# Performance work log

Measured on AMD Instinct MI355X. Metric: run time of the kernel, lower is better.

The kernel has to match this reference:

```python
import jax, jax.numpy as jnp
import numpy as np

N, E, D, K = 50000, 600000, 128, 8
EPS = 1e-09


def setup_inputs() -> dict:
    key = jax.random.key(0)
    ks = jax.random.split(key, 10)
    feature = jax.random.normal(ks[0], (N, D), dtype=jnp.float32)
    snorm_n = jax.random.uniform(ks[1], (N, 1), dtype=jnp.float32)
    src = jax.random.randint(ks[2], (E,), 0, N, dtype=jnp.int32)
    dst = jax.random.randint(ks[3], (E,), 0, N, dtype=jnp.int32)
    W_low = jax.random.normal(ks[4], (D, D), dtype=jnp.float32) / np.sqrt(D)
    W_high = jax.random.normal(ks[5], (D, D), dtype=jnp.float32) / np.sqrt(D)
    W_mid = jax.random.normal(ks[6], (D, D), dtype=jnp.float32) / np.sqrt(D)
    gamma_low = jax.random.uniform(ks[7], (K,), dtype=jnp.float32)
    gamma_high = jax.random.uniform(ks[8], (K,), dtype=jnp.float32)
    gamma_mid = jax.random.uniform(ks[9], (K,), dtype=jnp.float32)
    bias = jnp.zeros((D,), dtype=jnp.float32)
    return {"feature": feature, "snorm_n": snorm_n, "src": src, "dst": dst,
            "W_low": W_low, "W_high": W_high, "W_mid": W_mid,
            "gamma_low": gamma_low, "gamma_high": gamma_high,
            "gamma_mid": gamma_mid, "bias": bias}


def _mp(feat, src, dst, norm):
    # symmetric-normalized SpMM: h[v] = norm[v] * sum_{u->v} norm[u]*feat[u]
    msg = (feat * norm[:, None])[src]                        # [E, D] gather
    agg = jax.ops.segment_sum(msg, dst, num_segments=N)       # [N, D] scatter-add
    return agg * norm[:, None]


def reference(feature, snorm_n, src, dst, W_low, W_high, W_mid,
              gamma_low, gamma_high, gamma_mid, bias):
    deg = jax.ops.segment_sum(jnp.ones((E,), feature.dtype), dst, num_segments=N)
    norm = jnp.clip(deg, 1.0) ** -0.5                          # in-degree^-0.5
    alpha = jnp.linspace(EPS, 1.0 - EPS, K).astype(feature.dtype)
    midalpha = jnp.linspace(EPS, 1.0, K).astype(feature.dtype)

    h = _mp(feature, src, dst, norm)

    gl = jax.nn.relu(gamma_low)
    o0 = (jnp.dot(alpha, gl) * h + jnp.dot(1.0 - alpha, gl) * feature) @ W_low.T
    gh = jax.nn.relu(gamma_high)
    o1 = (jnp.dot(-alpha, gh) * h + jnp.dot(1.0 - alpha, gh) * feature) @ W_high.T
    gm = jax.nn.relu(gamma_mid)
    h1 = _mp(h, src, dst, norm)
    o2 = (jnp.sum(gm) * h1 - jnp.dot(midalpha, gm) * feature) @ W_mid.T

    # sequential mutual gating, exactly as the torch in-place updates
    o0 = o0 * jax.nn.sigmoid(o1 + o2)
    o1 = o1 * jax.nn.sigmoid(o0 + o2)
    o2 = o2 * jax.nn.sigmoid(o0 + o1)

    out = o0 + o1 + o2 + bias
    out = out * snorm_n          # graph_norm
    out = jax.nn.relu(out)       # activation
    return out
```

## Files before the change

kernel.cpp:

```cpp
#include <hip/hip_runtime.h>
#include <hip/hip_bf16.h>
#include <math.h>

#define N_NODES 50000
#define N_EDGES 600000
#define DIM 128
#define KGAM 8
#define EPSV 1e-9f

typedef __attribute__((ext_vector_type(8))) short short8;
typedef __attribute__((ext_vector_type(4))) float float4v;

__device__ __forceinline__ float bf2f(short s) {
    unsigned int u = ((unsigned int)(unsigned short)s) << 16;
    return __builtin_bit_cast(float, u);
}
__device__ __forceinline__ short f2bf(float f) {
    return (short)__builtin_bit_cast(unsigned short, __float2bfloat16(f));
}
__device__ __forceinline__ unsigned int pack2(float a, float b) {
    return (unsigned int)(unsigned short)f2bf(a) | ((unsigned int)(unsigned short)f2bf(b) << 16);
}
__device__ __forceinline__ float sigm(float x) { return 1.f / (1.f + __expf(-x)); }

__global__ void k_zero_int(int* __restrict__ p, int n) {
    int i = blockIdx.x * blockDim.x + threadIdx.x;
    if (i < n) p[i] = 0;
}

__global__ void k_deg(const int* __restrict__ dst, int* __restrict__ deg) {
    int e = blockIdx.x * blockDim.x + threadIdx.x;
    if (e < N_EDGES) atomicAdd(&deg[dst[e]], 1);
}

__global__ void k_scan1(const int* __restrict__ deg, int* __restrict__ rowstart,
                        int* __restrict__ bsums, float* __restrict__ norm) {
    __shared__ int s[256];
    int tid = threadIdx.x;
    int i0 = blockIdx.x * 1024 + tid * 4;
    int v[4]; int sum = 0;
#pragma unroll
    for (int c = 0; c < 4; ++c) {
        int i = i0 + c;
        int d = (i < N_NODES) ? deg[i] : 0;
        v[c] = d; sum += d;
    }
    s[tid] = sum; __syncthreads();
#pragma unroll
    for (int off = 1; off < 256; off <<= 1) {
        int t = (tid >= off) ? s[tid - off] : 0;
        __syncthreads();
        s[tid] += t;
        __syncthreads();
    }
    if (tid == 255) bsums[blockIdx.x] = s[255];
    int run = s[tid] - sum;
#pragma unroll
    for (int c = 0; c < 4; ++c) {
        int i = i0 + c;
        if (i < N_NODES) {
            rowstart[i] = run;
            norm[i] = rsqrtf((float)(v[c] < 1 ? 1 : v[c]));
        }
        run += v[c];
    }
}

__global__ void k_scan2(int* __restrict__ bsums, int nb) {
    __shared__ int s[64];
    int tid = threadIdx.x;
    int v = (tid < nb) ? bsums[tid] : 0;
    s[tid] = v; __syncthreads();
#pragma unroll
    for (int off = 1; off < 64; off <<= 1) {
        int t = (tid >= off) ? s[tid - off] : 0;
        __syncthreads();
        s[tid] += t;
        __syncthreads();
    }
    if (tid < nb) bsums[tid] = s[tid] - v;
}

__global__ void k_scan3(const int* __restrict__ bsums, int* __restrict__ rowstart) {
    int i = blockIdx.x * blockDim.x + threadIdx.x;
    if (i < N_NODES) rowstart[i] += bsums[i >> 10];
    if (i == 0) rowstart[N_NODES] = N_EDGES;
}

__global__ void k_fill(const int* __restrict__ src, const int* __restrict__ dst,
                       const int* __restrict__ rowstart, int* __restrict__ cnt,
                       int* __restrict__ esrc) {
    int e = blockIdx.x * blockDim.x + threadIdx.x;
    if (e < N_EDGES) {
        int d = dst[e];
        int slot = rowstart[d] + atomicAdd(&cnt[d], 1);
        esrc[slot] = src[e];
    }
}

__global__ void k_coeffs(const float* __restrict__ gl, const float* __restrict__ gh,
                         const float* __restrict__ gm, float* __restrict__ c) {
    if (threadIdx.x == 0 && blockIdx.x == 0) {
        float a0 = 0, b0 = 0, a1 = 0, b1 = 0, sg = 0, m2 = 0;
        for (int k = 0; k < KGAM; ++k) {
            float al = EPSV + (float)k * (1.f - 2.f * EPSV) / (KGAM - 1);
            float md = EPSV + (float)k * (1.f - EPSV) / (KGAM - 1);
            float l = fmaxf(gl[k], 0.f), h = fmaxf(gh[k], 0.f), m = fmaxf(gm[k], 0.f);
            a0 += al * l;  b0 += (1.f - al) * l;
            a1 += -al * h; b1 += (1.f - al) * h;
            sg += m;       m2 += md * m;
        }
        c[0] = a0; c[1] = b0; c[2] = a1; c[3] = b1; c[4] = sg; c[5] = -m2;
    }
}

__global__ void k_wconv(const float* __restrict__ W0, const float* __restrict__ W1,
                        const float* __restrict__ W2, unsigned int* __restrict__ Wb) {
    const float* Ws = (blockIdx.y == 0) ? W0 : (blockIdx.y == 1) ? W1 : W2;
    int i = (blockIdx.x * 256 + threadIdx.x) * 4;
    if (i < DIM * DIM) {
        float4 v = *(const float4*)(Ws + i);
        uint2 o; o.x = pack2(v.x, v.y); o.y = pack2(v.z, v.w);
        *(uint2*)(Wb + (blockIdx.y * DIM * DIM + i) / 2) = o;
    }
}

__global__ void k_prescale(const float4* __restrict__ f, const float* __restrict__ norm,
                           uint2* __restrict__ fb, uint2* __restrict__ fp) {
    int i = blockIdx.x * 256 + threadIdx.x;
    if (i >= N_NODES * DIM / 4) return;
    int row = i >> 5;
    float nv = norm[row];
    float4 v = f[i];
    uint2 a; a.x = pack2(v.x, v.y); a.y = pack2(v.z, v.w);
    uint2 b; b.x = pack2(v.x * nv, v.y * nv); b.y = pack2(v.z * nv, v.w * nv);
    fb[i] = a;
    fp[i] = b;
}

__device__ __forceinline__ void acc4(float4& a, uint2 r) {
    a.x += __builtin_bit_cast(float, r.x << 16);
    a.y += __builtin_bit_cast(float, r.x & 0xffff0000u);
    a.z += __builtin_bit_cast(float, r.y << 16);
    a.w += __builtin_bit_cast(float, r.y & 0xffff0000u);
}

__global__ void k_spmm(const uint2* __restrict__ in, const float* __restrict__ norm,
                       const int* __restrict__ rowstart, const int* __restrict__ esrc,
                       uint2* __restrict__ hout, uint2* __restrict__ preout, int wpre) {
    int v = blockIdx.x * 8 + (threadIdx.x >> 5);
    int l = threadIdx.x & 31;
    if (v >= N_NODES) return;
    int beg = rowstart[v], end = rowstart[v + 1];
    float4 acc = {0.f, 0.f, 0.f, 0.f};
    int t = beg;
    for (; t + 3 < end; t += 4) {
        int u0 = esrc[t], u1 = esrc[t + 1], u2 = esrc[t + 2], u3 = esrc[t + 3];
        uint2 r0 = in[(size_t)u0 * 32 + l];
        uint2 r1 = in[(size_t)u1 * 32 + l];
        uint2 r2 = in[(size_t)u2 * 32 + l];
        uint2 r3 = in[(size_t)u3 * 32 + l];
        acc4(acc, r0); acc4(acc, r1); acc4(acc, r2); acc4(acc, r3);
    }
    for (; t < end; ++t) {
        uint2 r = in[(size_t)esrc[t] * 32 + l];
        acc4(acc, r);
    }
    float nv = norm[v];
    float hx = acc.x * nv, hy = acc.y * nv, hz = acc.z * nv, hw = acc.w * nv;
    uint2 o; o.x = pack2(hx, hy); o.y = pack2(hz, hw);
    hout[(size_t)v * 32 + l] = o;
    if (wpre) {
        uint2 p; p.x = pack2(hx * nv, hy * nv); p.y = pack2(hz * nv, hw * nv);
        preout[(size_t)v * 32 + l] = p;
    }
}

#define RT 64
#define TSTR 136

__global__ __launch_bounds__(512, 4) void k_gemm_fused(
    const short* __restrict__ hB, const short* __restrict__ fB,
    const short* __restrict__ h1B, const short* __restrict__ Wb,
    const float* __restrict__ coeffs, const float* __restrict__ bias,
    const float* __restrict__ snorm, float* __restrict__ out) {
    __shared__ short Ts[3][RT * TSTR];

    const float c0 = coeffs[0], c1 = coeffs[1], c2 = coeffs[2];
    const float c3 = coeffs[3], c4 = coeffs[4], c5 = coeffs[5];
    const int r0 = blockIdx.x * RT;
    const int tid = threadIdx.x;

#pragma unroll
    for (int it = 0; it < 2; ++it) {
        int idx = tid + it * 512;
        int r = idx >> 4;
        int cg = (idx & 15) * 8;
        int row = r0 + r;
        short8 hv = {0,0,0,0,0,0,0,0}, fv = {0,0,0,0,0,0,0,0}, h1v = {0,0,0,0,0,0,0,0};
        if (row < N_NODES) {
            size_t base = (size_t)row * DIM + cg;
            hv  = *(const short8*)(hB + base);
            fv  = *(const short8*)(fB + base);
            h1v = *(const short8*)(h1B + base);
        }
        short8 t0, t1, t2;
#pragma unroll
        for (int j = 0; j < 8; ++j) {
            float hf = bf2f(hv[j]), ff = bf2f(fv[j]), h1f = bf2f(h1v[j]);
            t0[j] = f2bf(c0 * hf + c1 * ff);
            t1[j] = f2bf(c2 * hf + c3 * ff);
            t2[j] = f2bf(c4 * h1f + c5 * ff);
        }
        int la = r * TSTR + cg;
        *(short8*)&Ts[0][la] = t0;
        *(short8*)&Ts[1][la] = t1;
        *(short8*)&Ts[2][la] = t2;
    }
    __syncthreads();

    const int lane = tid & 63;
    const int ct = tid >> 6;
    const int m = lane & 15;
    const int quad = lane >> 4;

    float4v acc[3][4];
    const float4v zero = {0.f, 0.f, 0.f, 0.f};
#pragma unroll
    for (int g = 0; g < 3; ++g)
#pragma unroll
        for (int rt = 0; rt < 4; ++rt) acc[g][rt] = zero;

    const short* wbase = Wb + (ct * 16 + m) * DIM + quad * 8;
#pragma unroll
    for (int ks = 0; ks < 4; ++ks) {
        const short* wp = wbase + ks * 32;
        short8 b0 = *(const short8*)(wp);
        short8 b1 = *(const short8*)(wp + DIM * DIM);
        short8 b2 = *(const short8*)(wp + 2 * DIM * DIM);
#pragma unroll
        for (int rt = 0; rt < 4; ++rt) {
            int aoff = (rt * 16 + m) * TSTR + ks * 32 + quad * 8;
            short8 a0 = *(const short8*)&Ts[0][aoff];
            short8 a1 = *(const short8*)&Ts[1][aoff];
            short8 a2 = *(const short8*)&Ts[2][aoff];
            acc[0][rt] = __builtin_amdgcn_mfma_f32_16x16x32_bf16(a0, b0, acc[0][rt], 0, 0, 0);
            acc[1][rt] = __builtin_amdgcn_mfma_f32_16x16x32_bf16(a1, b1, acc[1][rt], 0, 0, 0);
            acc[2][rt] = __builtin_amdgcn_mfma_f32_16x16x32_bf16(a2, b2, acc[2][rt], 0, 0, 0);
        }
    }

    const int col = ct * 16 + m;
    const float bc = bias[col];
#pragma unroll
    for (int rt = 0; rt < 4; ++rt) {
#pragma unroll
        for (int r = 0; r < 4; ++r) {
            int row = r0 + rt * 16 + quad * 4 + r;
            if (row < N_NODES) {
                float sn = snorm[row];
                float o0 = acc[0][rt][r], o1 = acc[1][rt][r], o2 = acc[2][rt][r];
                float g0 = o0 * sigm(o1 + o2);
                float g1 = o1 * sigm(g0 + o2);
                float g2 = o2 * sigm(g0 + g1);
                float vv = (g0 + g1 + g2 + bc) * sn;
                out[(size_t)row * DIM + col] = fmaxf(vv, 0.f);
            }
        }
    }
}

extern "C" void kernel_launch(void* const* d_in, const int* in_sizes, int n_in,
                              void* d_out, int out_size, void* d_ws, size_t ws_size,
                              hipStream_t stream) {
    const float* feature = (const float*)d_in[0];
    const float* snorm   = (const float*)d_in[1];
    const int*   src     = (const int*)d_in[2];
    const int*   dst     = (const int*)d_in[3];
    const float* W_low   = (const float*)d_in[4];
    const float* W_high  = (const float*)d_in[5];
    const float* W_mid   = (const float*)d_in[6];
    const float* gl      = (const float*)d_in[7];
    const float* gh      = (const float*)d_in[8];
    const float* gm      = (const float*)d_in[9];
    const float* bias    = (const float*)d_in[10];
    float* out = (float*)d_out;

    char* w = (char*)d_ws;
    auto alloc = [&](size_t bytes) {
        char* p = w;
        w += (bytes + 255) & ~(size_t)255;
        return p;
    };
    float* norm   = (float*)alloc((size_t)N_NODES * 4);
    int* deg      = (int*)alloc((size_t)2 * N_NODES * 4);
    int* cnt      = deg + N_NODES;
    int* rowstart = (int*)alloc((size_t)(N_NODES + 1) * 4);
    int* bsums    = (int*)alloc(64 * 4);
    int* esrc     = (int*)alloc((size_t)N_EDGES * 4);
    float* coeffs = (float*)alloc(64 * 4);
    short* Wb     = (short*)alloc((size_t)3 * DIM * DIM * 2);
    short* fb     = (short*)alloc((size_t)N_NODES * DIM * 2);
    short* fp     = (short*)alloc((size_t)N_NODES * DIM * 2);
    short* h      = (short*)alloc((size_t)N_NODES * DIM * 2);
    short* hp     = (short*)alloc((size_t)N_NODES * DIM * 2);
    short* h1     = (short*)alloc((size_t)N_NODES * DIM * 2);

    k_zero_int<<<(2 * N_NODES + 255) / 256, 256, 0, stream>>>(deg, 2 * N_NODES);
    k_deg<<<(N_EDGES + 255) / 256, 256, 0, stream>>>(dst, deg);
    int nchunks = (N_NODES + 1023) / 1024;
    k_scan1<<<nchunks, 256, 0, stream>>>(deg, rowstart, bsums, norm);
    k_scan2<<<1, 64, 0, stream>>>(bsums, nchunks);
    k_scan3<<<(N_NODES + 255) / 256, 256, 0, stream>>>(bsums, rowstart);
    k_fill<<<(N_EDGES + 255) / 256, 256, 0, stream>>>(src, dst, rowstart, cnt, esrc);
    k_coeffs<<<1, 1, 0, stream>>>(gl, gh, gm, coeffs);
    k_wconv<<<dim3(16, 3), 256, 0, stream>>>(W_low, W_high, W_mid, (unsigned int*)Wb);
    k_prescale<<<(N_NODES * DIM / 4 + 255) / 256, 256, 0, stream>>>(
        (const float4*)feature, norm, (uint2*)fb, (uint2*)fp);

    int spmm_blocks = (N_NODES + 7) / 8;
    k_spmm<<<spmm_blocks, 256, 0, stream>>>((const uint2*)fp, norm, rowstart, esrc,
                                            (uint2*)h, (uint2*)hp, 1);
    k_spmm<<<spmm_blocks, 256, 0, stream>>>((const uint2*)hp, norm, rowstart, esrc,
                                            (uint2*)h1, (uint2*)hp, 0);

    k_gemm_fused<<<(N_NODES + RT - 1) / RT, 512, 0, stream>>>(
        h, fb, h1, Wb, coeffs, bias, snorm, out);
}
```

Measured before the change: 254.3 us.

## Fuse prep kernels, store edge norms in CSR records, widen SpMM gathers

Merges the zeroing, weight conversion, coefficient and feature bf16 conversion into one prep kernel. The scan3 pass is removed by adding block sums at use sites, and cnt is zeroed inside scan1. Each CSR entry now stores the source node's norm next to its index, so the SpMM scales on the fly and the separate prescaled feature and hp buffers are no longer needed. SpMM uses 16 lanes per node with 16-byte loads. In exchange the edge records double in size and each edge needs an extra FMA per element.

```diff
diff --git a/kernel.cpp b/kernel.cpp
--- a/kernel.cpp
+++ b/kernel.cpp
@@ -22,85 +22,35 @@
     return (unsigned int)(unsigned short)f2bf(a) | ((unsigned int)(unsigned short)f2bf(b) << 16);
 }
 __device__ __forceinline__ float sigm(float x) { return 1.f / (1.f + __expf(-x)); }
-
-__global__ void k_zero_int(int* __restrict__ p, int n) {
-    int i = blockIdx.x * blockDim.x + threadIdx.x;
-    if (i < n) p[i] = 0;
-}
-
-__global__ void k_deg(const int* __restrict__ dst, int* __restrict__ deg) {
-    int e = blockIdx.x * blockDim.x + threadIdx.x;
-    if (e < N_EDGES) atomicAdd(&deg[dst[e]], 1);
-}
-
-__global__ void k_scan1(const int* __restrict__ deg, int* __restrict__ rowstart,
-                        int* __restrict__ bsums, float* __restrict__ norm) {
-    __shared__ int s[256];
-    int tid = threadIdx.x;
-    int i0 = blockIdx.x * 1024 + tid * 4;
-    int v[4]; int sum = 0;
-#pragma unroll
-    for (int c = 0; c < 4; ++c) {
-        int i = i0 + c;
-        int d = (i < N_NODES) ? deg[i] : 0;
-        v[c] = d; sum += d;
-    }
-    s[tid] = sum; __syncthreads();
-#pragma unroll
-    for (int off = 1; off < 256; off <<= 1) {
-        int t = (tid >= off) ? s[tid - off] : 0;
-        __syncthreads();
-        s[tid] += t;
-        __syncthreads();
-    }
-    if (tid == 255) bsums[blockIdx.x] = s[255];
-    int run = s[tid] - sum;
-#pragma unroll
-    for (int c = 0; c < 4; ++c) {
-        int i = i0 + c;
-        if (i < N_NODES) {
-            rowstart[i] = run;
-            norm[i] = rsqrtf((float)(v[c] < 1 ? 1 : v[c]));
-        }
-        run += v[c];
-    }
-}
-
-__global__ void k_scan2(int* __restrict__ bsums, int nb) {
-    __shared__ int s[64];
-    int tid = threadIdx.x;
-    int v = (tid < nb) ? bsums[tid] : 0;
-    s[tid] = v; __syncthreads();
-#pragma unroll
-    for (int off = 1; off < 64; off <<= 1) {
-        int t = (tid >= off) ? s[tid - off] : 0;
-        __syncthreads();
-        s[tid] += t;
-        __syncthreads();
-    }
-    if (tid < nb) bsums[tid] = s[tid] - v;
-}
-
-__global__ void k_scan3(const int* __restrict__ bsums, int* __restrict__ rowstart) {
-    int i = blockIdx.x * blockDim.x + threadIdx.x;
-    if (i < N_NODES) rowstart[i] += bsums[i >> 10];
-    if (i == 0) rowstart[N_NODES] = N_EDGES;
-}
-
-__global__ void k_fill(const int* __restrict__ src, const int* __restrict__ dst,
-                       const int* __restrict__ rowstart, int* __restrict__ cnt,
-                       int* __restrict__ esrc) {
-    int e = blockIdx.x * blockDim.x + threadIdx.x;
-    if (e < N_EDGES) {
-        int d = dst[e];
-        int slot = rowstart[d] + atomicAdd(&cnt[d], 1);
-        esrc[slot] = src[e];
-    }
-}
-
-__global__ void k_coeffs(const float* __restrict__ gl, const float* __restrict__ gh,
-                         const float* __restrict__ gm, float* __restrict__ c) {
-    if (threadIdx.x == 0 && blockIdx.x == 0) {
+__device__ __forceinline__ float ulo(unsigned int u) { return __builtin_bit_cast(float, u << 16); }
+__device__ __forceinline__ float uhi(unsigned int u) { return __builtin_bit_cast(float, u & 0xffff0000u); }
+
+__global__ void k_prep(const float4* __restrict__ feat4,
+                       const float* __restrict__ W0, const float* __restrict__ W1,
+                       const float* __restrict__ W2,
+                       const float* __restrict__ gl, const float* __restrict__ gh,
+                       const float* __restrict__ gm,
+                       uint4* __restrict__ fb4, unsigned int* __restrict__ Wb,
+                       float* __restrict__ coeffs, int* __restrict__ deg) {
+    int b = blockIdx.x, tid = threadIdx.x;
+    if (b < 3125) {
+        int idx = b * 256 + tid;
+        if (idx < N_NODES) deg[idx] = 0;
+        float4 v0 = feat4[idx * 2];
+        float4 v1 = feat4[idx * 2 + 1];
+        uint4 o;
+        o.x = pack2(v0.x, v0.y); o.y = pack2(v0.z, v0.w);
+        o.z = pack2(v1.x, v1.y); o.w = pack2(v1.z, v1.w);
+        fb4[idx] = o;
+    } else if (b < 3173) {
+        int j = (b - 3125) * 256 + tid;
+        int g = j >> 12;
+        int i = (j & 4095) * 4;
+        const float* Ws = (g == 0) ? W0 : (g == 1) ? W1 : W2;
+        float4 v = *(const float4*)(Ws + i);
+        uint2 o; o.x = pack2(v.x, v.y); o.y = pack2(v.z, v.w);
+        *(uint2*)(Wb + (g * DIM * DIM + i) / 2) = o;
+    } else if (tid == 0) {
         float a0 = 0, b0 = 0, a1 = 0, b1 = 0, sg = 0, m2 = 0;
         for (int k = 0; k < KGAM; ++k) {
             float al = EPSV + (float)k * (1.f - 2.f * EPSV) / (KGAM - 1);
@@ -110,70 +60,123 @@
             a1 += -al * h; b1 += (1.f - al) * h;
             sg += m;       m2 += md * m;
         }
-        c[0] = a0; c[1] = b0; c[2] = a1; c[3] = b1; c[4] = sg; c[5] = -m2;
-    }
-}
-
-__global__ void k_wconv(const float* __restrict__ W0, const float* __restrict__ W1,
-                        const float* __restrict__ W2, unsigned int* __restrict__ Wb) {
-    const float* Ws = (blockIdx.y == 0) ? W0 : (blockIdx.y == 1) ? W1 : W2;
-    int i = (blockIdx.x * 256 + threadIdx.x) * 4;
-    if (i < DIM * DIM) {
-        float4 v = *(const float4*)(Ws + i);
-        uint2 o; o.x = pack2(v.x, v.y); o.y = pack2(v.z, v.w);
-        *(uint2*)(Wb + (blockIdx.y * DIM * DIM + i) / 2) = o;
-    }
-}
-
-__global__ void k_prescale(const float4* __restrict__ f, const float* __restrict__ norm,
-                           uint2* __restrict__ fb, uint2* __restrict__ fp) {
-    int i = blockIdx.x * 256 + threadIdx.x;
-    if (i >= N_NODES * DIM / 4) return;
-    int row = i >> 5;
-    float nv = norm[row];
-    float4 v = f[i];
-    uint2 a; a.x = pack2(v.x, v.y); a.y = pack2(v.z, v.w);
-    uint2 b; b.x = pack2(v.x * nv, v.y * nv); b.y = pack2(v.z * nv, v.w * nv);
-    fb[i] = a;
-    fp[i] = b;
-}
-
-__device__ __forceinline__ void acc4(float4& a, uint2 r) {
-    a.x += __builtin_bit_cast(float, r.x << 16);
-    a.y += __builtin_bit_cast(float, r.x & 0xffff0000u);
-    a.z += __builtin_bit_cast(float, r.y << 16);
-    a.w += __builtin_bit_cast(float, r.y & 0xffff0000u);
-}
-
-__global__ void k_spmm(const uint2* __restrict__ in, const float* __restrict__ norm,
-                       const int* __restrict__ rowstart, const int* __restrict__ esrc,
-                       uint2* __restrict__ hout, uint2* __restrict__ preout, int wpre) {
-    int v = blockIdx.x * 8 + (threadIdx.x >> 5);
-    int l = threadIdx.x & 31;
-    if (v >= N_NODES) return;
-    int beg = rowstart[v], end = rowstart[v + 1];
-    float4 acc = {0.f, 0.f, 0.f, 0.f};
+        coeffs[0] = a0; coeffs[1] = b0; coeffs[2] = a1;
+        coeffs[3] = b1; coeffs[4] = sg; coeffs[5] = -m2;
+    }
+}
+
+__global__ void k_deg(const int* __restrict__ dst, int* __restrict__ deg) {
+    int e = blockIdx.x * blockDim.x + threadIdx.x;
+    if (e < N_EDGES) atomicAdd(&deg[dst[e]], 1);
+}
+
+__global__ void k_scan1(const int* __restrict__ deg, int* __restrict__ rowstart,
+                        int* __restrict__ bsums, float* __restrict__ norm,
+                        int* __restrict__ cnt) {
+    __shared__ int s[256];
+    int tid = threadIdx.x;
+    int i0 = blockIdx.x * 1024 + tid * 4;
+    int v[4]; int sum = 0;
+#pragma unroll
+    for (int c = 0; c < 4; ++c) {
+        int i = i0 + c;
+        int d = (i < N_NODES) ? deg[i] : 0;
+        v[c] = d; sum += d;
+    }
+    s[tid] = sum; __syncthreads();
+#pragma unroll
+    for (int off = 1; off < 256; off <<= 1) {
+        int t = (tid >= off) ? s[tid - off] : 0;
+        __syncthreads();
+        s[tid] += t;
+        __syncthreads();
+    }
+    if (tid == 255) bsums[blockIdx.x] = s[255];
+    int run = s[tid] - sum;
+#pragma unroll
+    for (int c = 0; c < 4; ++c) {
+        int i = i0 + c;
+        if (i < N_NODES) {
+            rowstart[i] = run;
+            norm[i] = rsqrtf((float)(v[c] < 1 ? 1 : v[c]));
+            cnt[i] = 0;
+        }
+        run += v[c];
+    }
+}
+
+__global__ void k_scan2(int* __restrict__ bsums, int nb) {
+    __shared__ int s[64];
+    int tid = threadIdx.x;
+    int v = (tid < nb) ? bsums[tid] : 0;
+    s[tid] = v; __syncthreads();
+#pragma unroll
+    for (int off = 1; off < 64; off <<= 1) {
+        int t = (tid >= off) ? s[tid - off] : 0;
+        __syncthreads();
+        s[tid] += t;
+        __syncthreads();
+    }
+    if (tid < nb) bsums[tid] = s[tid] - v;
+}
+
+__global__ void k_fill(const int* __restrict__ src, const int* __restrict__ dst,
+                       const int* __restrict__ rowstart, const int* __restrict__ bsums,
+                       int* __restrict__ cnt, const float* __restrict__ norm,
+                       uint2* __restrict__ er) {
+    int e = blockIdx.x * blockDim.x + threadIdx.x;
+    if (e < N_EDGES) {
+        int d = dst[e];
+        int slot = rowstart[d] + bsums[d >> 10] + atomicAdd(&cnt[d], 1);
+        int u = src[e];
+        uint2 rec;
+        rec.x = (unsigned int)u;
+        rec.y = __builtin_bit_cast(unsigned int, norm[u]);
+        er[slot] = rec;
+    }
+}
+
+__device__ __forceinline__ void acc8(float4v& a0, float4v& a1, uint4 r, float nu) {
+    a0.x = fmaf(nu, ulo(r.x), a0.x); a0.y = fmaf(nu, uhi(r.x), a0.y);
+    a0.z = fmaf(nu, ulo(r.y), a0.z); a0.w = fmaf(nu, uhi(r.y), a0.w);
+    a1.x = fmaf(nu, ulo(r.z), a1.x); a1.y = fmaf(nu, uhi(r.z), a1.y);
+    a1.z = fmaf(nu, ulo(r.w), a1.z); a1.w = fmaf(nu, uhi(r.w), a1.w);
+}
+
+__global__ __launch_bounds__(512) void k_spmm(
+    const uint4* __restrict__ in, const float* __restrict__ norm,
+    const int* __restrict__ rowstart, const int* __restrict__ bsums,
+    const uint2* __restrict__ er, uint4* __restrict__ out) {
+    int node = blockIdx.x * 32 + (threadIdx.x >> 4);
+    if (node >= N_NODES) return;
+    int gl = threadIdx.x & 15;
+    int beg = rowstart[node] + bsums[node >> 10];
+    int end = (node == N_NODES - 1) ? N_EDGES
+                                    : rowstart[node + 1] + bsums[(node + 1) >> 10];
+    float4v a0 = {0.f, 0.f, 0.f, 0.f};
+    float4v a1 = {0.f, 0.f, 0.f, 0.f};
     int t = beg;
     for (; t + 3 < end; t += 4) {
-        int u0 = esrc[t], u1 = esrc[t + 1], u2 = esrc[t + 2], u3 = esrc[t + 3];
-        uint2 r0 = in[(size_t)u0 * 32 + l];
-        uint2 r1 = in[(size_t)u1 * 32 + l];
-        uint2 r2 = in[(size_t)u2 * 32 + l];
-        uint2 r3 = in[(size_t)u3 * 32 + l];
-        acc4(acc, r0); acc4(acc, r1); acc4(acc, r2); acc4(acc, r3);
+        uint2 e0 = er[t], e1 = er[t + 1], e2 = er[t + 2], e3 = er[t + 3];
+        uint4 r0 = in[e0.x * 16u + gl];
+        uint4 r1 = in[e1.x * 16u + gl];
+        uint4 r2 = in[e2.x * 16u + gl];
+        uint4 r3 = in[e3.x * 16u + gl];
+        acc8(a0, a1, r0, __builtin_bit_cast(float, e0.y));
+        acc8(a0, a1, r1, __builtin_bit_cast(float, e1.y));
+        acc8(a0, a1, r2, __builtin_bit_cast(float, e2.y));
+        acc8(a0, a1, r3, __builtin_bit_cast(float, e3.y));
     }
     for (; t < end; ++t) {
-        uint2 r = in[(size_t)esrc[t] * 32 + l];
-        acc4(acc, r);
-    }
-    float nv = norm[v];
-    float hx = acc.x * nv, hy = acc.y * nv, hz = acc.z * nv, hw = acc.w * nv;
-    uint2 o; o.x = pack2(hx, hy); o.y = pack2(hz, hw);
-    hout[(size_t)v * 32 + l] = o;
-    if (wpre) {
-        uint2 p; p.x = pack2(hx * nv, hy * nv); p.y = pack2(hz * nv, hw * nv);
-        preout[(size_t)v * 32 + l] = p;
-    }
+        uint2 e = er[t];
+        uint4 r = in[e.x * 16u + gl];
+        acc8(a0, a1, r, __builtin_bit_cast(float, e.y));
+    }
+    float nv = norm[node];
+    uint4 o;
+    o.x = pack2(a0.x * nv, a0.y * nv); o.y = pack2(a0.z * nv, a0.w * nv);
+    o.z = pack2(a1.x * nv, a1.y * nv); o.w = pack2(a1.z * nv, a1.w * nv);
+    out[node * 16u + gl] = o;
 }
 
 #define RT 64
@@ -293,37 +296,32 @@
         return p;
     };
     float* norm   = (float*)alloc((size_t)N_NODES * 4);
-    int* deg      = (int*)alloc((size_t)2 * N_NODES * 4);
-    int* cnt      = deg + N_NODES;
+    int* deg      = (int*)alloc((size_t)N_NODES * 4);
+    int* cnt      = (int*)alloc((size_t)N_NODES * 4);
     int* rowstart = (int*)alloc((size_t)(N_NODES + 1) * 4);
     int* bsums    = (int*)alloc(64 * 4);
-    int* esrc     = (int*)alloc((size_t)N_EDGES * 4);
+    uint2* er     = (uint2*)alloc((size_t)N_EDGES * 8);
     float* coeffs = (float*)alloc(64 * 4);
     short* Wb     = (short*)alloc((size_t)3 * DIM * DIM * 2);
     short* fb     = (short*)alloc((size_t)N_NODES * DIM * 2);
-    short* fp     = (short*)alloc((size_t)N_NODES * DIM * 2);
     short* h      = (short*)alloc((size_t)N_NODES * DIM * 2);
-    short* hp     = (short*)alloc((size_t)N_NODES * DIM * 2);
     short* h1     = (short*)alloc((size_t)N_NODES * DIM * 2);
 
-    k_zero_int<<<(2 * N_NODES + 255) / 256, 256, 0, stream>>>(deg, 2 * N_NODES);
+    const int nchunks = (N_NODES + 1023) / 1024;
+
+    k_prep<<<3125 + 48 + 1, 256, 0, stream>>>(
+        (const float4*)feature, W_low, W_high, W_mid, gl, gh, gm,
+        (uint4*)fb, (unsigned int*)Wb, coeffs, deg);
     k_deg<<<(N_EDGES + 255) / 256, 256, 0, stream>>>(dst, deg);
-    int nchunks = (N_NODES + 1023) / 1024;
-    k_scan1<<<nchunks, 256, 0, stream>>>(deg, rowstart, bsums, norm);
+    k_scan1<<<nchunks, 256, 0, stream>>>(deg, rowstart, bsums, norm, cnt);
     k_scan2<<<1, 64, 0, stream>>>(bsums, nchunks);
-    k_scan3<<<(N_NODES + 255) / 256, 256, 0, stream>>>(bsums, rowstart);
-    k_fill<<<(N_EDGES + 255) / 256, 256, 0, stream>>>(src, dst, rowstart, cnt, esrc);
-    k_coeffs<<<1, 1, 0, stream>>>(gl, gh, gm, coeffs);
-    k_wconv<<<dim3(16, 3), 256, 0, stream>>>(W_low, W_high, W_mid, (unsigned int*)Wb);
-    k_prescale<<<(N_NODES * DIM / 4 + 255) / 256, 256, 0, stream>>>(
-        (const float4*)feature, norm, (uint2*)fb, (uint2*)fp);
-
-    int spmm_blocks = (N_NODES + 7) / 8;
-    k_spmm<<<spmm_blocks, 256, 0, stream>>>((const uint2*)fp, norm, rowstart, esrc,
-                                            (uint2*)h, (uint2*)hp, 1);
-    k_spmm<<<spmm_blocks, 256, 0, stream>>>((const uint2*)hp, norm, rowstart, esrc,
-                                            (uint2*)h1, (uint2*)hp, 0);
-
+    k_fill<<<(N_EDGES + 255) / 256, 256, 0, stream>>>(src, dst, rowstart, bsums,
+                                                      cnt, norm, er);
+    int spmm_blocks = (N_NODES + 31) / 32;
+    k_spmm<<<spmm_blocks, 512, 0, stream>>>((const uint4*)fb, norm, rowstart, bsums,
+                                            er, (uint4*)h);
+    k_spmm<<<spmm_blocks, 512, 0, stream>>>((const uint4*)h, norm, rowstart, bsums,
+                                            er, (uint4*)h1);
     k_gemm_fused<<<(N_NODES + RT - 1) / RT, 512, 0, stream>>>(
         h, fb, h1, Wb, coeffs, bias, snorm, out);
 }
```

Result: faster. 240.0 us (-5.6%).
